# Kernel tuning notes

Measured on AMD Instinct MI355X. Metric: run time of the kernel, lower is better.

Reference implementation:

```python
import jax, jax.numpy as jnp
import numpy as np

NB_CLASSES = 10
EPS = 1e-8  # torch cosine_similarity eps


def gcn_conv(x, W, b, src, dst, n):
    h = x @ W
    deg = jax.ops.segment_sum(jnp.ones_like(src, dtype=h.dtype), dst, num_segments=n) + 1.0
    dinv = deg ** -0.5
    coef = (dinv[src] * dinv[dst])[:, None]
    agg = jax.ops.segment_sum(h[src] * coef, dst, num_segments=n)
    return agg + h * (1.0 / deg)[:, None] + b


def condition_net(e, w_in, b_in, w_hid, b_hid, w_out, b_out):
    # ConditionNet with num_layers=2: input_fc -> elu -> hidden_fc[0] -> elu -> output_fc
    h = jax.nn.elu(e @ w_in + b_in)
    h = jax.nn.elu(h @ w_hid + b_hid)
    return h @ w_out + b_out


def setup_inputs() -> dict:
    key = jax.random.key(0)
    N, E, D, H, T, M = 20000, 320000, 256, 256, 3, 2048
    ks = jax.random.split(key, 24)
    s = 1.0 / np.sqrt(D)
    inp = {
        "x": jax.random.normal(ks[0], (N, D), dtype=jnp.float32),
        "src": jax.random.randint(ks[1], (E,), 0, N, dtype=jnp.int32),
        "dst": jax.random.randint(ks[2], (E,), 0, N, dtype=jnp.int32),
        "idx": jax.random.randint(ks[3], (M,), 0, N, dtype=jnp.int32),
        "labels": jax.random.randint(ks[4], (M,), 0, NB_CLASSES, dtype=jnp.int32),
        "train": 1,
        # 3 GCNConv layers (all D->D, residual structure forces equal widths)
        "gcn_W1": jax.random.normal(ks[5], (D, D), dtype=jnp.float32) * s,
        "gcn_b1": jnp.zeros((D,), dtype=jnp.float32),
        "gcn_W2": jax.random.normal(ks[6], (D, D), dtype=jnp.float32) * s,
        "gcn_b2": jnp.zeros((D,), dtype=jnp.float32),
        "gcn_W3": jax.random.normal(ks[7], (D, D), dtype=jnp.float32) * s,
        "gcn_b3": jnp.zeros((D,), dtype=jnp.float32),
        # T=3 ConditionNets, params stacked on leading axis
        "cn_w_in": jax.random.normal(ks[8], (T, D, H), dtype=jnp.float32) * s,
        "cn_b_in": jnp.zeros((T, H), dtype=jnp.float32),
        "cn_w_hid": jax.random.normal(ks[9], (T, H, H), dtype=jnp.float32) * s,
        "cn_b_hid": jnp.zeros((T, H), dtype=jnp.float32),
        "cn_w_out": jax.random.normal(ks[10], (T, H, D), dtype=jnp.float32) * s,
        "cn_b_out": jnp.zeros((T, D), dtype=jnp.float32),
        # Embed_prompt
        "p_list": jax.random.normal(ks[11], (5, D), dtype=jnp.float32) * s,
        "a_W": jax.random.normal(ks[12], (D, 5), dtype=jnp.float32) * s,
        "a_b": jnp.zeros((5,), dtype=jnp.float32),
        # gcn_weight2 (trainable); weight1 and weight3 are frozen zeros, closed over
        "gcn_weight2": jnp.float32(1.0),
    }
    return inp


def reference(x, src, dst, idx, labels, train,
              gcn_W1, gcn_b1, gcn_W2, gcn_b2, gcn_W3, gcn_b3,
              cn_w_in, cn_b_in, cn_w_hid, cn_b_hid, cn_w_out, cn_b_out,
              p_list, a_W, a_b, gcn_weight2):
    n = x.shape[0]
    origin_x = x
    w1 = jnp.float32(0.0)  # gcn_weight1 (frozen)
    w3 = jnp.float32(0.0)  # gcn_weight3 (frozen)
    T = cn_w_in.shape[0]
    for t in range(T):  # think layers (small static count)
        e1 = gcn_conv(x, gcn_W1, gcn_b1, src, dst, n)
        e2 = gcn_conv(e1, gcn_W2, gcn_b2, src, dst, n) + e1
        e3 = gcn_conv(e2, gcn_W3, gcn_b3, src, dst, n) + e2
        embed = w1 * e1 + gcn_weight2 * e2 + w3 * e3
        prompt = condition_net(embed, cn_w_in[t], cn_b_in[t], cn_w_hid[t], cn_b_hid[t],
                               cn_w_out[t], cn_b_out[t])
        x = prompt * origin_x
    # full gcn(x, edge_index): 3 convs with ELU activation (standard GCN forward)
    h = jax.nn.elu(gcn_conv(x, gcn_W1, gcn_b1, src, dst, n))
    h = jax.nn.elu(gcn_conv(h, gcn_W2, gcn_b2, src, dst, n))
    h = jax.nn.elu(gcn_conv(h, gcn_W3, gcn_b3, src, dst, n))
    # Embed_prompt: attention over 5 learned prompt vectors
    weight = jax.nn.softmax(h @ a_W + a_b, axis=1)  # [N, 5]
    embed = h + weight @ p_list
    rawret = embed[idx]  # [M, D]
    # train==1: class prototypes via scatter-mean over labels
    sums = jax.ops.segment_sum(rawret, labels, num_segments=NB_CLASSES)
    counts = jax.ops.segment_sum(jnp.ones_like(labels, dtype=rawret.dtype), labels,
                                 num_segments=NB_CLASSES)
    ave = sums / jnp.maximum(counts, 1.0)[:, None]  # [C, D]
    # fused cosine similarity: normalize both, one matmul (replaces M*C scalar loop)
    rn = rawret / jnp.maximum(jnp.linalg.norm(rawret, axis=1, keepdims=True), EPS)
    an = ave / jnp.maximum(jnp.linalg.norm(ave, axis=1, keepdims=True), EPS)
    ret = jax.nn.softmax(rn @ an.T, axis=1)  # [M, C]
    return ret
```

## Files before the change

kernel.cpp:

```cpp
#include <hip/hip_runtime.h>
#include <hip/hip_bf16.h>
#include <math.h>

#define NN 20000
#define DD 256
#define EE 320000
#define MM 2048
#define CC 10
#define TT 3

typedef __attribute__((ext_vector_type(8))) short s8v;
typedef __attribute__((ext_vector_type(4))) float f4v;

__device__ unsigned short g_xb[NN * DD];
__device__ unsigned short g_xo[NN * DD];
__device__ unsigned short g_hb[NN * DD];
__device__ unsigned short g_e1b[NN * DD];
__device__ unsigned short g_e2b[NN * DD];
__device__ int   g_cnt[NN];
__device__ int   g_cursor[NN];
__device__ int   g_rowstart[NN + 1];
__device__ float g_dinv[NN];
__device__ float g_invdeg[NN];
__device__ int   g_part[128];
__device__ int2  g_edge[EE];
__device__ float g_sums[CC * DD];
__device__ float g_cntf[CC];
__device__ unsigned short g_wT1[12 * DD * DD];
__device__ unsigned short g_wT2[12 * DD * DD];

__device__ __forceinline__ float wave_sum(float v) {
#pragma unroll
  for (int off = 32; off > 0; off >>= 1) v += __shfl_xor(v, off);
  return v;
}

__device__ __forceinline__ float eluf(float x) {
  return x > 0.f ? x : expm1f(x);
}

__device__ __forceinline__ float bf2f(unsigned short u) {
  union { unsigned int i; float f; } c;
  c.i = (unsigned int)u << 16;
  return c.f;
}

__device__ __forceinline__ float2 bfpair(unsigned int d) {
  union { unsigned int i; float f; } a, b;
  a.i = d << 16;
  b.i = d & 0xffff0000u;
  return make_float2(a.f, b.f);
}

__device__ __forceinline__ unsigned int packbf(float x, float y) {
  union { __hip_bfloat162 v; unsigned int u; } c;
  c.v = __float22bfloat162_rn(make_float2(x, y));
  return c.u;
}

__device__ __forceinline__ void gl_lds16(const unsigned short* g, unsigned short* l) {
  __builtin_amdgcn_global_load_lds(
      (const __attribute__((address_space(1))) unsigned int*)g,
      (__attribute__((address_space(3))) unsigned int*)l, 16, 0, 0);
}

struct WPtrs { const float* p[12]; };

__global__ __launch_bounds__(256) void init_k(const float* __restrict__ x,
                                              unsigned short* __restrict__ xb,
                                              WPtrs wp) {
  __shared__ float t[64][65];
  int b = blockIdx.x;
  int tid = threadIdx.x;
  if (b < 2500) {
    int i = b * 256 + tid;
    const float4* x4 = (const float4*)x;
    float4 a = x4[i * 2], bb = x4[i * 2 + 1];
    uint4 o;
    o.x = packbf(a.x, a.y);
    o.y = packbf(a.z, a.w);
    o.z = packbf(bb.x, bb.y);
    o.w = packbf(bb.z, bb.w);
    ((uint4*)xb)[i] = o;
  } else if (b < 2692) {
    int bb = b - 2500;
    int widx = bb >> 4;
    int rem = bb & 15;
    int kt0 = (rem >> 2) * 64, nt0 = (rem & 3) * 64;
    const float* W = wp.p[widx];
    int ln = tid & 63, lk = tid >> 6;
    for (int kk = lk; kk < 64; kk += 4)
      t[kk][ln] = W[(size_t)(kt0 + kk) * DD + nt0 + ln];
    __syncthreads();
    for (int nn = lk; nn < 64; nn += 4) {
      float v = t[ln][nn];
      __hip_bfloat16 hb = __float2bfloat16(v);
      float hf = __bfloat162float(hb);
      __hip_bfloat16 lb = __float2bfloat16(v - hf);
      union { __hip_bfloat16 b; unsigned short s; } ch, cl;
      ch.b = hb; cl.b = lb;
      size_t o = (size_t)widx * DD * DD + (size_t)(nt0 + nn) * DD + kt0 + ln;
      g_wT1[o] = ch.s;
      g_wT2[o] = cl.s;
    }
  } else {
    int i = (b - 2692) * 256 + tid;
    if (i < NN) { g_cnt[i] = 0; g_cursor[i] = 0; }
    if (i < CC * DD) g_sums[i] = 0.f;
    if (i < CC) g_cntf[i] = 0.f;
  }
}

__global__ void hist_k(const int* __restrict__ dst) {
  int e = blockIdx.x * blockDim.x + threadIdx.x;
  if (e < EE) atomicAdd(&g_cnt[dst[e]], 1);
}

__global__ __launch_bounds__(256) void scanA_k() {
  __shared__ int s[256];
  int t = threadIdx.x;
  int i = blockIdx.x * 256 + t;
  int v = (i < NN) ? g_cnt[i] : 0;
  s[t] = v;
  __syncthreads();
#pragma unroll
  for (int off = 128; off > 0; off >>= 1) {
    if (t < off) s[t] += s[t + off];
    __syncthreads();
  }
  if (t == 0) g_part[blockIdx.x] = s[0];
}

__global__ __launch_bounds__(256) void scanC_k() {
  __shared__ int ps[128];
  __shared__ int s[256];
  int t = threadIdx.x;
  if (t < 128) ps[t] = (t < 79) ? g_part[t] : 0;
  __syncthreads();
#pragma unroll
  for (int off = 1; off < 128; off <<= 1) {
    int v = (t >= off && t < 128) ? ps[t - off] : 0;
    __syncthreads();
    if (t < 128) ps[t] += v;
    __syncthreads();
  }
  int base = (blockIdx.x == 0) ? 0 : ps[blockIdx.x - 1];
  int i = blockIdx.x * 256 + t;
  int v = (i < NN) ? g_cnt[i] : 0;
  s[t] = v;
  __syncthreads();
#pragma unroll
  for (int off = 1; off < 256; off <<= 1) {
    int x2 = (t >= off) ? s[t - off] : 0;
    __syncthreads();
    s[t] += x2;
    __syncthreads();
  }
  if (i < NN) {
    g_rowstart[i] = base + s[t] - v;
    float dg = (float)(v + 1);
    g_invdeg[i] = 1.0f / dg;
    g_dinv[i] = 1.0f / sqrtf(dg);
  }
  if (blockIdx.x == 78 && t == 0) g_rowstart[NN] = EE;
}

__global__ void fill_k(const int* __restrict__ src, const int* __restrict__ dst) {
  int e = blockIdx.x * blockDim.x + threadIdx.x;
  if (e < EE) {
    int d = dst[e];
    int p = atomicAdd(&g_cursor[d], 1);
    int j = g_rowstart[d] + p;
    int si = src[e];
    float coef = g_dinv[si] * g_dinv[d];
    g_edge[j] = make_int2(si * 512, __float_as_int(coef));
  }
}

template <int SPLIT>
union GemmSM {
  unsigned short st[2][(1024 + 512 * SPLIT) * 8];
  float ct[64][68];
};

template <int EPI, int SPLIT>
__global__ __launch_bounds__(256) void gemm_k(const unsigned short* __restrict__ A,
                                              const unsigned short* __restrict__ B1,
                                              const unsigned short* __restrict__ B2,
                                              unsigned short* __restrict__ C,
                                              const float* __restrict__ bias,
                                              const float* __restrict__ alphap,
                                              const unsigned short* __restrict__ mul) {
  __shared__ GemmSM<SPLIT> sm;
  constexpr int CB = 1024 + 512 * SPLIT;
  int b = blockIdx.x;
  int xcd = b & 7, off = b >> 3;
  int logical = (xcd < 4) ? xcd * 157 + off : 628 + (xcd - 4) * 156 + off;
  int mblk = logical >> 2, nblk = logical & 3;
  int row0 = mblk * 64, col0 = nblk * 64;

  int tid = threadIdx.x;
  int wv = tid >> 6, lane = tid & 63;
  int wm = wv >> 1, wn = wv & 1;
  int lr = lane & 15, lk = lane >> 4;

  f4v acc[2][2];
#pragma unroll
  for (int i = 0; i < 2; ++i)
#pragma unroll
    for (int j = 0; j < 2; ++j) acc[i][j] = (f4v){0.f, 0.f, 0.f, 0.f};

  auto stage = [&](int buf, int kt) {
    unsigned short* base = sm.st[buf];
#pragma unroll
    for (int i = 0; i < CB / 256; ++i) {
      int cb = (wv * (CB / 256) + i) * 64;
      int c = cb + lane;
      unsigned short* ldst = base + (size_t)cb * 8;
      if (c < 512) {
        int row = c >> 3, pos = c & 7;
        int kc = pos ^ (row & 7);
        int gr = row0 + row;
        gr = gr < NN ? gr : NN - 1;
        gl_lds16(A + (size_t)gr * DD + kt + kc * 8, ldst);
      } else if (c < 1024) {
        int c2 = c - 512;
        int col = c2 >> 3, pos = c2 & 7;
        int kc = pos ^ (col & 7);
        gl_lds16(B1 + (size_t)(col0 + col) * DD + kt + kc * 8, ldst);
      } else {
        int c2 = c - 1024;
        int col = c2 >> 3, pos = c2 & 7;
        int kc = pos ^ (col & 7);
        gl_lds16(B2 + (size_t)(col0 + col) * DD + kt + kc * 8, ldst);
      }
    }
  };

  stage(0, 0);
  __syncthreads();

  int buf = 0;
#pragma unroll
  for (int t = 0; t < 4; ++t) {
    if (t < 3) stage(buf ^ 1, (t + 1) * 64);
    const unsigned short* base = sm.st[buf];
#pragma unroll
    for (int ksub = 0; ksub < 2; ++ksub) {
      int kc = ksub * 4 + lk;
      s8v a[2], b1v[2], b2v[2];
#pragma unroll
      for (int mi = 0; mi < 2; ++mi) {
        int row = wm * 32 + mi * 16 + lr;
        a[mi] = *(const s8v*)(base + (row * 8 + (kc ^ (row & 7))) * 8);
      }
#pragma unroll
      for (int nj = 0; nj < 2; ++nj) {
        int col = wn * 32 + nj * 16 + lr;
        int ch = col * 8 + (kc ^ (col & 7));
        b1v[nj] = *(const s8v*)(base + (512 + ch) * 8);
        if (SPLIT) b2v[nj] = *(const s8v*)(base + (1024 + ch) * 8);
      }
#pragma unroll
      for (int mi = 0; mi < 2; ++mi)
#pragma unroll
        for (int nj = 0; nj < 2; ++nj) {
          acc[mi][nj] = __builtin_amdgcn_mfma_f32_16x16x32_bf16(a[mi], b1v[nj], acc[mi][nj], 0, 0, 0);
          if (SPLIT)
            acc[mi][nj] = __builtin_amdgcn_mfma_f32_16x16x32_bf16(a[mi], b2v[nj], acc[mi][nj], 0, 0, 0);
        }
    }
    __syncthreads();
    buf ^= 1;
  }

#pragma unroll
  for (int mi = 0; mi < 2; ++mi)
#pragma unroll
    for (int nj = 0; nj < 2; ++nj)
#pragma unroll
      for (int r = 0; r < 4; ++r)
        sm.ct[wm * 32 + mi * 16 + lk * 4 + r][wn * 32 + nj * 16 + lr] = acc[mi][nj][r];
  __syncthreads();

  float alpha = 1.f;
  if (EPI == 1) alpha = alphap ? *alphap : 1.f;
#pragma unroll
  for (int p = 0; p < 2; ++p) {
    int row = p * 32 + (tid >> 3);
    int c0 = (tid & 7) * 8;
    int gr = row0 + row;
    int gc = col0 + c0;
    if (gr < NN) {
      float v[8];
      float4 va = *(float4*)&sm.ct[row][c0];
      float4 vb = *(float4*)&sm.ct[row][c0 + 4];
      v[0] = va.x; v[1] = va.y; v[2] = va.z; v[3] = va.w;
      v[4] = vb.x; v[5] = vb.y; v[6] = vb.z; v[7] = vb.w;
      if (EPI == 1) {
        float4 bv0 = *(const float4*)(bias + gc);
        float4 bv1 = *(const float4*)(bias + gc + 4);
        float bb[8] = {bv0.x, bv0.y, bv0.z, bv0.w, bv1.x, bv1.y, bv1.z, bv1.w};
#pragma unroll
        for (int i = 0; i < 8; ++i) v[i] = eluf(fmaf(alpha, v[i], bb[i]));
      } else if (EPI == 2) {
        float4 bv0 = *(const float4*)(bias + gc);
        float4 bv1 = *(const float4*)(bias + gc + 4);
        float bb[8] = {bv0.x, bv0.y, bv0.z, bv0.w, bv1.x, bv1.y, bv1.z, bv1.w};
        uint4 mu = *(const uint4*)(mul + (size_t)gr * DD + gc);
        float2 m0 = bfpair(mu.x), m1 = bfpair(mu.y), m2 = bfpair(mu.z), m3 = bfpair(mu.w);
        float mm[8] = {m0.x, m0.y, m1.x, m1.y, m2.x, m2.y, m3.x, m3.y};
#pragma unroll
        for (int i = 0; i < 8; ++i) v[i] = (v[i] + bb[i]) * mm[i];
      }
      uint4 o;
      o.x = packbf(v[0], v[1]);
      o.y = packbf(v[2], v[3]);
      o.z = packbf(v[4], v[5]);
      o.w = packbf(v[6], v[7]);
      *(uint4*)(C + (size_t)gr * DD + gc) = o;
    }
  }
}

template <int RES>
__device__ __forceinline__ void agg_row8(int row, int sl, int hf,
                                         const unsigned short* __restrict__ h,
                                         const float* __restrict__ bias,
                                         const unsigned short* __restrict__ res,
                                         float* o) {
  const char* hb = (const char*)h;
  int lo = sl * 16;
  float acc[8];
#pragma unroll
  for (int k = 0; k < 8; ++k) acc[k] = 0.f;
  int s = g_rowstart[row], e = g_rowstart[row + 1];
  int j = s;
  for (; j + 12 <= e; j += 12) {
    int2 E[6];
    uint4 V[6];
#pragma unroll
    for (int u = 0; u < 6; ++u) E[u] = g_edge[j + 2 * u + hf];
#pragma unroll
    for (int u = 0; u < 6; ++u) V[u] = *(const uint4*)(hb + (size_t)E[u].x + lo);
#pragma unroll
    for (int u = 0; u < 6; ++u) {
      float c = __int_as_float(E[u].y);
      float2 p0 = bfpair(V[u].x), p1 = bfpair(V[u].y);
      float2 p2 = bfpair(V[u].z), p3 = bfpair(V[u].w);
      acc[0] = fmaf(c, p0.x, acc[0]); acc[1] = fmaf(c, p0.y, acc[1]);
      acc[2] = fmaf(c, p1.x, acc[2]); acc[3] = fmaf(c, p1.y, acc[3]);
      acc[4] = fmaf(c, p2.x, acc[4]); acc[5] = fmaf(c, p2.y, acc[5]);
      acc[6] = fmaf(c, p3.x, acc[6]); acc[7] = fmaf(c, p3.y, acc[7]);
    }
  }
  for (; j < e; j += 2) {
    int jj = j + hf;
    int jc = jj < e ? jj : e - 1;
    int2 E0 = g_edge[jc];
    uint4 V0 = *(const uint4*)(hb + (size_t)E0.x + lo);
    float c = (jj < e) ? __int_as_float(E0.y) : 0.f;
    float2 p0 = bfpair(V0.x), p1 = bfpair(V0.y);
    float2 p2 = bfpair(V0.z), p3 = bfpair(V0.w);
    acc[0] = fmaf(c, p0.x, acc[0]); acc[1] = fmaf(c, p0.y, acc[1]);
    acc[2] = fmaf(c, p1.x, acc[2]); acc[3] = fmaf(c, p1.y, acc[3]);
    acc[4] = fmaf(c, p2.x, acc[4]); acc[5] = fmaf(c, p2.y, acc[5]);
    acc[6] = fmaf(c, p3.x, acc[6]); acc[7] = fmaf(c, p3.y, acc[7]);
  }
#pragma unroll
  for (int k = 0; k < 8; ++k) acc[k] += __shfl_xor(acc[k], 32);
  float idg = g_invdeg[row];
  uint4 hv = *(const uint4*)(hb + (size_t)row * 512 + lo);
  float2 h0 = bfpair(hv.x), h1 = bfpair(hv.y), h2 = bfpair(hv.z), h3 = bfpair(hv.w);
  float hw[8] = {h0.x, h0.y, h1.x, h1.y, h2.x, h2.y, h3.x, h3.y};
  float4 b0 = *(const float4*)(bias + sl * 8);
  float4 b1 = *(const float4*)(bias + sl * 8 + 4);
  float bb[8] = {b0.x, b0.y, b0.z, b0.w, b1.x, b1.y, b1.z, b1.w};
#pragma unroll
  for (int k = 0; k < 8; ++k) o[k] = acc[k] + hw[k] * idg + bb[k];
  if (RES) {
    uint4 rv = *(const uint4*)((const char*)res + (size_t)row * 512 + lo);
    float2 r0 = bfpair(rv.x), r1 = bfpair(rv.y), r2 = bfpair(rv.z), r3 = bfpair(rv.w);
    float rw[8] = {r0.x, r0.y, r1.x, r1.y, r2.x, r2.y, r3.x, r3.y};
#pragma unroll
    for (int k = 0; k < 8; ++k) o[k] += rw[k];
  }
}

template <int ELU, int RES>
__global__ __launch_bounds__(256) void agg_k(const unsigned short* __restrict__ h,
                                             const float* __restrict__ bias,
                                             const unsigned short* __restrict__ res,
                                             unsigned short* __restrict__ out) {
  int row = (blockIdx.x * 256 + threadIdx.x) >> 6;
  int lane = threadIdx.x & 63;
  int sl = lane & 31, hf = lane >> 5;
  float o[8];
  agg_row8<RES>(row, sl, hf, h, bias, res, o);
  if (ELU) {
#pragma unroll
    for (int k = 0; k < 8; ++k) o[k] = eluf(o[k]);
  }
  if (hf == 0) {
    uint4 pk;
    pk.x = packbf(o[0], o[1]);
    pk.y = packbf(o[2], o[3]);
    pk.z = packbf(o[4], o[5]);
    pk.w = packbf(o[6], o[7]);
    *(uint4*)((char*)out + (size_t)row * 512 + sl * 16) = pk;
  }
}

__global__ __launch_bounds__(256) void aggattn_k(const unsigned short* __restrict__ h,
                                                 const float* __restrict__ bias,
                                                 const float* __restrict__ aW,
                                                 const float* __restrict__ ab,
                                                 const float* __restrict__ plist,
                                                 unsigned short* __restrict__ out) {
  int row = (blockIdx.x * 256 + threadIdx.x) >> 6;
  int lane = threadIdx.x & 63;
  int sl = lane & 31, hf = lane >> 5;
  float o[8];
  agg_row8<0>(row, sl, hf, h, bias, nullptr, o);
#pragma unroll
  for (int k = 0; k < 8; ++k) o[k] = eluf(o[k]);
  int c0 = sl * 8;
  float lg[5];
#pragma unroll
  for (int k = 0; k < 5; ++k) {
    float p = 0.f;
#pragma unroll
    for (int i = 0; i < 8; ++i) p = fmaf(o[i], aW[(c0 + i) * 5 + k], p);
    lg[k] = wave_sum(p) * 0.5f + ab[k];
  }
  float mx = lg[0];
#pragma unroll
  for (int k = 1; k < 5; ++k) mx = fmaxf(mx, lg[k]);
  float w[5], sum = 0.f;
#pragma unroll
  for (int k = 0; k < 5; ++k) { w[k] = expf(lg[k] - mx); sum += w[k]; }
  float inv = 1.f / sum;
#pragma unroll
  for (int k = 0; k < 5; ++k) {
    float wk = w[k] * inv;
    float4 p0 = *(const float4*)(plist + k * DD + c0);
    float4 p1 = *(const float4*)(plist + k * DD + c0 + 4);
    o[0] = fmaf(wk, p0.x, o[0]); o[1] = fmaf(wk, p0.y, o[1]);
    o[2] = fmaf(wk, p0.z, o[2]); o[3] = fmaf(wk, p0.w, o[3]);
    o[4] = fmaf(wk, p1.x, o[4]); o[5] = fmaf(wk, p1.y, o[5]);
    o[6] = fmaf(wk, p1.z, o[6]); o[7] = fmaf(wk, p1.w, o[7]);
  }
  if (hf == 0) {
    uint4 pk;
    pk.x = packbf(o[0], o[1]);
    pk.y = packbf(o[2], o[3]);
    pk.z = packbf(o[4], o[5]);
    pk.w = packbf(o[6], o[7]);
    *(uint4*)((char*)out + (size_t)row * 512 + sl * 16) = pk;
  }
}

__global__ __launch_bounds__(256) void proto_k(const unsigned short* __restrict__ embed,
                                               const int* __restrict__ idxp,
                                               const int* __restrict__ labels) {
  __shared__ float sums[CC][DD];
  __shared__ float cnts[CC];
  int t = threadIdx.x;
#pragma unroll
  for (int c = 0; c < CC; ++c) sums[c][t] = 0.f;
  if (t < CC) cnts[t] = 0.f;
  __syncthreads();
  int m0 = blockIdx.x * 32;
  for (int r0 = 0; r0 < 32; r0 += 4) {
    int i4[4], l4[4];
    float v[4];
#pragma unroll
    for (int u = 0; u < 4; ++u) {
      int m = m0 + r0 + u;
      i4[u] = idxp[m];
      l4[u] = labels[m];
    }
#pragma unroll
    for (int u = 0; u < 4; ++u) v[u] = bf2f(embed[(size_t)i4[u] * DD + t]);
#pragma unroll
    for (int u = 0; u < 4; ++u) sums[l4[u]][t] += v[u];
    if (t == 0) {
#pragma unroll
      for (int u = 0; u < 4; ++u) cnts[l4[u]] += 1.f;
    }
  }
  __syncthreads();
#pragma unroll
  for (int c = 0; c < CC; ++c) atomicAdd(&g_sums[c * DD + t], sums[c][t]);
  if (t < CC) atomicAdd(&g_cntf[t], cnts[t]);
}

__global__ __launch_bounds__(256) void cos_k(const unsigned short* __restrict__ embed,
                                             const int* __restrict__ idxp,
                                             float* __restrict__ out) {
  __shared__ float an[CC][DD];
  __shared__ float red[4];
  int t = threadIdx.x;
  int lane = t & 63, wv = t >> 6;
  for (int c = 0; c < CC; ++c) {
    float v = g_sums[c * DD + t] / fmaxf(g_cntf[c], 1.0f);
    float sq = wave_sum(v * v);
    if (lane == 0) red[wv] = sq;
    __syncthreads();
    float tot = red[0] + red[1] + red[2] + red[3];
    float nrm = fmaxf(sqrtf(tot), 1e-8f);
    an[c][t] = v / nrm;
    __syncthreads();
  }
  int wid = (blockIdx.x * 256 + t) >> 6;
  if (wid >= MM) return;
  int row = idxp[wid];
  uint2 rv = ((const uint2*)embed)[(size_t)row * 64 + lane];
  float2 r0 = bfpair(rv.x), r1 = bfpair(rv.y);
  float4 r = make_float4(r0.x, r0.y, r1.x, r1.y);
  float n = wave_sum(r.x * r.x + r.y * r.y + r.z * r.z + r.w * r.w);
  float rnf = 1.0f / fmaxf(sqrtf(n), 1e-8f);
  float lg[CC];
#pragma unroll
  for (int c = 0; c < CC; ++c) {
    float4 a = ((const float4*)&an[c][0])[lane];
    float p = r.x * a.x + r.y * a.y + r.z * a.z + r.w * a.w;
    lg[c] = wave_sum(p) * rnf;
  }
  float mx = lg[0];
#pragma unroll
  for (int c = 1; c < CC; ++c) mx = fmaxf(mx, lg[c]);
  float s = 0.f, w[CC];
#pragma unroll
  for (int c = 0; c < CC; ++c) { w[c] = expf(lg[c] - mx); s += w[c]; }
  float inv = 1.f / s;
#pragma unroll
  for (int c = 0; c < CC; ++c)
    if (lane == c) out[(size_t)wid * CC + c] = w[c] * inv;
}

extern "C" void kernel_launch(void* const* d_in, const int* in_sizes, int n_in,
                              void* d_out, int out_size, void* d_ws, size_t ws_size,
                              hipStream_t stream) {
  (void)in_sizes; (void)n_in; (void)d_ws; (void)ws_size; (void)out_size;
  const float* x      = (const float*)d_in[0];
  const int*   src    = (const int*)d_in[1];
  const int*   dst    = (const int*)d_in[2];
  const int*   idx    = (const int*)d_in[3];
  const int*   labels = (const int*)d_in[4];
  const float* W1 = (const float*)d_in[6];
  const float* b1 = (const float*)d_in[7];
  const float* W2 = (const float*)d_in[8];
  const float* b2 = (const float*)d_in[9];
  const float* W3 = (const float*)d_in[10];
  const float* b3 = (const float*)d_in[11];
  const float* cw_in  = (const float*)d_in[12];
  const float* cb_in  = (const float*)d_in[13];
  const float* cw_hid = (const float*)d_in[14];
  const float* cb_hid = (const float*)d_in[15];
  const float* cw_out = (const float*)d_in[16];
  const float* cb_out = (const float*)d_in[17];
  const float* plist  = (const float*)d_in[18];
  const float* aW     = (const float*)d_in[19];
  const float* ab     = (const float*)d_in[20];
  const float* w2s    = (const float*)d_in[21];
  float* out = (float*)d_out;

  unsigned short *xb, *xo, *hb, *e1b, *e2b, *wt1, *wt2;
  hipGetSymbolAddress((void**)&xb,  HIP_SYMBOL(g_xb));
  hipGetSymbolAddress((void**)&xo,  HIP_SYMBOL(g_xo));
  hipGetSymbolAddress((void**)&hb,  HIP_SYMBOL(g_hb));
  hipGetSymbolAddress((void**)&e1b, HIP_SYMBOL(g_e1b));
  hipGetSymbolAddress((void**)&e2b, HIP_SYMBOL(g_e2b));
  hipGetSymbolAddress((void**)&wt1, HIP_SYMBOL(g_wT1));
  hipGetSymbolAddress((void**)&wt2, HIP_SYMBOL(g_wT2));

  auto WT1 = [&](int w) { return (const unsigned short*)(wt1 + (size_t)w * DD * DD); };
  auto WT2 = [&](int w) { return (const unsigned short*)(wt2 + (size_t)w * DD * DD); };

  WPtrs wp;
  wp.p[0] = W1; wp.p[1] = W2; wp.p[2] = W3;
  for (int t = 0; t < 3; ++t) {
    wp.p[3 + t] = cw_in  + (size_t)t * DD * DD;
    wp.p[6 + t] = cw_hid + (size_t)t * DD * DD;
    wp.p[9 + t] = cw_out + (size_t)t * DD * DD;
  }
  init_k<<<2771, 256, 0, stream>>>(x, xb, wp);
  hist_k<<<1250, 256, 0, stream>>>(dst);
  scanA_k<<<79, 256, 0, stream>>>();
  scanC_k<<<79, 256, 0, stream>>>();
  fill_k<<<1250, 256, 0, stream>>>(src, dst);

  const int GG = 1252;
  const unsigned short* xin = xb;
  for (int t = 0; t < TT; ++t) {
    gemm_k<0, 1><<<GG, 256, 0, stream>>>(xin, WT1(0), WT2(0), hb, nullptr, nullptr, nullptr);
    agg_k<0, 0><<<5000, 256, 0, stream>>>(hb, b1, nullptr, e1b);
    gemm_k<0, 1><<<GG, 256, 0, stream>>>(e1b, WT1(1), WT2(1), hb, nullptr, nullptr, nullptr);
    agg_k<0, 1><<<5000, 256, 0, stream>>>(hb, b2, e1b, e2b);
    gemm_k<1, 0><<<GG, 256, 0, stream>>>(e2b, WT1(3 + t), WT1(3 + t), e1b,
                                         cb_in + (size_t)t * DD, w2s, nullptr);
    gemm_k<1, 0><<<GG, 256, 0, stream>>>(e1b, WT1(6 + t), WT1(6 + t), hb,
                                         cb_hid + (size_t)t * DD, nullptr, nullptr);
    gemm_k<2, 0><<<GG, 256, 0, stream>>>(hb, WT1(9 + t), WT1(9 + t), xo,
                                         cb_out + (size_t)t * DD, nullptr, xb);
    xin = xo;
  }

  gemm_k<0, 1><<<GG, 256, 0, stream>>>(xin, WT1(0), WT2(0), hb, nullptr, nullptr, nullptr);
  agg_k<1, 0><<<5000, 256, 0, stream>>>(hb, b1, nullptr, e1b);
  gemm_k<0, 1><<<GG, 256, 0, stream>>>(e1b, WT1(1), WT2(1), hb, nullptr, nullptr, nullptr);
  agg_k<1, 0><<<5000, 256, 0, stream>>>(hb, b2, nullptr, e2b);
  gemm_k<0, 1><<<GG, 256, 0, stream>>>(e2b, WT1(2), WT2(2), hb, nullptr, nullptr, nullptr);
  aggattn_k<<<5000, 256, 0, stream>>>(hb, b3, aW, ab, plist, e2b);

  proto_k<<<64, 256, 0, stream>>>(e2b, idx, labels);
  cos_k<<<512, 256, 0, stream>>>(e2b, idx, out);
}
```

Before: 539.3 us.

## Slice GCN aggregation by feature columns and apply prompt attention only to sampled rows

New measurement: 1.017 ms. 1.89x slower.

```diff
diff --git a/kernel.cpp b/kernel.cpp
--- a/kernel.cpp
+++ b/kernel.cpp
@@ -37,12 +37,6 @@
 
 __device__ __forceinline__ float eluf(float x) {
   return x > 0.f ? x : expm1f(x);
-}
-
-__device__ __forceinline__ float bf2f(unsigned short u) {
-  union { unsigned int i; float f; } c;
-  c.i = (unsigned int)u << 16;
-  return c.f;
 }
 
 __device__ __forceinline__ float2 bfpair(unsigned int d) {
@@ -323,115 +317,91 @@
   }
 }
 
-template <int RES>
-__device__ __forceinline__ void agg_row8(int row, int sl, int hf,
-                                         const unsigned short* __restrict__ h,
-                                         const float* __restrict__ bias,
-                                         const unsigned short* __restrict__ res,
-                                         float* o) {
-  const char* hb = (const char*)h;
-  int lo = sl * 16;
-  float acc[8];
-#pragma unroll
-  for (int k = 0; k < 8; ++k) acc[k] = 0.f;
-  int s = g_rowstart[row], e = g_rowstart[row + 1];
-  int j = s;
-  for (; j + 12 <= e; j += 12) {
-    int2 E[6];
-    uint4 V[6];
-#pragma unroll
-    for (int u = 0; u < 6; ++u) E[u] = g_edge[j + 2 * u + hf];
-#pragma unroll
-    for (int u = 0; u < 6; ++u) V[u] = *(const uint4*)(hb + (size_t)E[u].x + lo);
-#pragma unroll
-    for (int u = 0; u < 6; ++u) {
-      float c = __int_as_float(E[u].y);
-      float2 p0 = bfpair(V[u].x), p1 = bfpair(V[u].y);
-      float2 p2 = bfpair(V[u].z), p3 = bfpair(V[u].w);
-      acc[0] = fmaf(c, p0.x, acc[0]); acc[1] = fmaf(c, p0.y, acc[1]);
-      acc[2] = fmaf(c, p1.x, acc[2]); acc[3] = fmaf(c, p1.y, acc[3]);
-      acc[4] = fmaf(c, p2.x, acc[4]); acc[5] = fmaf(c, p2.y, acc[5]);
-      acc[6] = fmaf(c, p3.x, acc[6]); acc[7] = fmaf(c, p3.y, acc[7]);
-    }
-  }
-  for (; j < e; j += 2) {
-    int jj = j + hf;
-    int jc = jj < e ? jj : e - 1;
-    int2 E0 = g_edge[jc];
-    uint4 V0 = *(const uint4*)(hb + (size_t)E0.x + lo);
-    float c = (jj < e) ? __int_as_float(E0.y) : 0.f;
-    float2 p0 = bfpair(V0.x), p1 = bfpair(V0.y);
-    float2 p2 = bfpair(V0.z), p3 = bfpair(V0.w);
-    acc[0] = fmaf(c, p0.x, acc[0]); acc[1] = fmaf(c, p0.y, acc[1]);
-    acc[2] = fmaf(c, p1.x, acc[2]); acc[3] = fmaf(c, p1.y, acc[3]);
-    acc[4] = fmaf(c, p2.x, acc[4]); acc[5] = fmaf(c, p2.y, acc[5]);
-    acc[6] = fmaf(c, p3.x, acc[6]); acc[7] = fmaf(c, p3.y, acc[7]);
-  }
-#pragma unroll
-  for (int k = 0; k < 8; ++k) acc[k] += __shfl_xor(acc[k], 32);
-  float idg = g_invdeg[row];
-  uint4 hv = *(const uint4*)(hb + (size_t)row * 512 + lo);
-  float2 h0 = bfpair(hv.x), h1 = bfpair(hv.y), h2 = bfpair(hv.z), h3 = bfpair(hv.w);
-  float hw[8] = {h0.x, h0.y, h1.x, h1.y, h2.x, h2.y, h3.x, h3.y};
-  float4 b0 = *(const float4*)(bias + sl * 8);
-  float4 b1 = *(const float4*)(bias + sl * 8 + 4);
-  float bb[8] = {b0.x, b0.y, b0.z, b0.w, b1.x, b1.y, b1.z, b1.w};
-#pragma unroll
-  for (int k = 0; k < 8; ++k) o[k] = acc[k] + hw[k] * idg + bb[k];
-  if (RES) {
-    uint4 rv = *(const uint4*)((const char*)res + (size_t)row * 512 + lo);
-    float2 r0 = bfpair(rv.x), r1 = bfpair(rv.y), r2 = bfpair(rv.z), r3 = bfpair(rv.w);
-    float rw[8] = {r0.x, r0.y, r1.x, r1.y, r2.x, r2.y, r3.x, r3.y};
-#pragma unroll
-    for (int k = 0; k < 8; ++k) o[k] += rw[k];
-  }
-}
-
 template <int ELU, int RES>
 __global__ __launch_bounds__(256) void agg_k(const unsigned short* __restrict__ h,
                                              const float* __restrict__ bias,
                                              const unsigned short* __restrict__ res,
                                              unsigned short* __restrict__ out) {
-  int row = (blockIdx.x * 256 + threadIdx.x) >> 6;
-  int lane = threadIdx.x & 63;
-  int sl = lane & 31, hf = lane >> 5;
-  float o[8];
-  agg_row8<RES>(row, sl, hf, h, bias, res, o);
-  if (ELU) {
-#pragma unroll
-    for (int k = 0; k < 8; ++k) o[k] = eluf(o[k]);
-  }
-  if (hf == 0) {
-    uint4 pk;
-    pk.x = packbf(o[0], o[1]);
-    pk.y = packbf(o[2], o[3]);
-    pk.z = packbf(o[4], o[5]);
-    pk.w = packbf(o[6], o[7]);
-    *(uint4*)((char*)out + (size_t)row * 512 + sl * 16) = pk;
-  }
-}
-
-__global__ __launch_bounds__(256) void aggattn_k(const unsigned short* __restrict__ h,
-                                                 const float* __restrict__ bias,
-                                                 const float* __restrict__ aW,
-                                                 const float* __restrict__ ab,
-                                                 const float* __restrict__ plist,
-                                                 unsigned short* __restrict__ out) {
-  int row = (blockIdx.x * 256 + threadIdx.x) >> 6;
-  int lane = threadIdx.x & 63;
-  int sl = lane & 31, hf = lane >> 5;
-  float o[8];
-  agg_row8<0>(row, sl, hf, h, bias, nullptr, o);
-#pragma unroll
-  for (int k = 0; k < 8; ++k) o[k] = eluf(o[k]);
-  int c0 = sl * 8;
+  int b = blockIdx.x;
+  int slice = b & 7, chunk = b >> 3;
+  int t = threadIdx.x;
+  int wv = t >> 6, lane = t & 63;
+  int g = lane >> 4, sl = lane & 15;
+  int lo = slice * 64 + sl * 4;
+  const char* hb8 = (const char*)h;
+  float2 bv = *(const float2*)(bias + slice * 32 + sl * 2);
+  int rbase = chunk * 64 + wv * 16;
+#pragma unroll 1
+  for (int rr = 0; rr < 16; ++rr) {
+    int row = rbase + rr;
+    if (row >= NN) break;
+    int s = g_rowstart[row], e = g_rowstart[row + 1];
+    float ax = 0.f, ay = 0.f;
+    int j = s;
+    for (; j + 16 <= e; j += 16) {
+      int2 E[4];
+      unsigned int V[4];
+#pragma unroll
+      for (int u = 0; u < 4; ++u) E[u] = g_edge[j + u * 4 + g];
+#pragma unroll
+      for (int u = 0; u < 4; ++u) V[u] = *(const unsigned int*)(hb8 + (size_t)E[u].x + lo);
+#pragma unroll
+      for (int u = 0; u < 4; ++u) {
+        float c = __int_as_float(E[u].y);
+        float2 p = bfpair(V[u]);
+        ax = fmaf(c, p.x, ax);
+        ay = fmaf(c, p.y, ay);
+      }
+    }
+    for (; j + 4 <= e; j += 4) {
+      int2 E0 = g_edge[j + g];
+      unsigned int V0 = *(const unsigned int*)(hb8 + (size_t)E0.x + lo);
+      float c = __int_as_float(E0.y);
+      float2 p = bfpair(V0);
+      ax = fmaf(c, p.x, ax);
+      ay = fmaf(c, p.y, ay);
+    }
+    if (j < e) {
+      int jj = j + g;
+      if (jj < e) {
+        int2 E0 = g_edge[jj];
+        unsigned int V0 = *(const unsigned int*)(hb8 + (size_t)E0.x + lo);
+        float c = __int_as_float(E0.y);
+        float2 p = bfpair(V0);
+        ax = fmaf(c, p.x, ax);
+        ay = fmaf(c, p.y, ay);
+      }
+    }
+    ax += __shfl_xor(ax, 16); ax += __shfl_xor(ax, 32);
+    ay += __shfl_xor(ay, 16); ay += __shfl_xor(ay, 32);
+    float idg = g_invdeg[row];
+    unsigned int hv = *(const unsigned int*)(hb8 + (size_t)row * 512 + lo);
+    float2 hp = bfpair(hv);
+    float ox = ax + hp.x * idg + bv.x;
+    float oy = ay + hp.y * idg + bv.y;
+    if (RES) {
+      unsigned int rv = *(const unsigned int*)((const char*)res + (size_t)row * 512 + lo);
+      float2 rp = bfpair(rv);
+      ox += rp.x;
+      oy += rp.y;
+    }
+    if (ELU) { ox = eluf(ox); oy = eluf(oy); }
+    if (g == 0)
+      *(unsigned int*)((char*)out + (size_t)row * 512 + lo) = packbf(ox, oy);
+  }
+}
+
+__device__ __forceinline__ float4 attn_apply(float4 r, int lane,
+                                             const float* __restrict__ aW,
+                                             const float* __restrict__ ab,
+                                             const float* __restrict__ plist) {
+  int d = lane * 4;
   float lg[5];
 #pragma unroll
   for (int k = 0; k < 5; ++k) {
-    float p = 0.f;
-#pragma unroll
-    for (int i = 0; i < 8; ++i) p = fmaf(o[i], aW[(c0 + i) * 5 + k], p);
-    lg[k] = wave_sum(p) * 0.5f + ab[k];
+    float p = r.x * aW[(d + 0) * 5 + k] + r.y * aW[(d + 1) * 5 + k] +
+              r.z * aW[(d + 2) * 5 + k] + r.w * aW[(d + 3) * 5 + k];
+    lg[k] = wave_sum(p) + ab[k];
   }
   float mx = lg[0];
 #pragma unroll
@@ -443,26 +413,21 @@
 #pragma unroll
   for (int k = 0; k < 5; ++k) {
     float wk = w[k] * inv;
-    float4 p0 = *(const float4*)(plist + k * DD + c0);
-    float4 p1 = *(const float4*)(plist + k * DD + c0 + 4);
-    o[0] = fmaf(wk, p0.x, o[0]); o[1] = fmaf(wk, p0.y, o[1]);
-    o[2] = fmaf(wk, p0.z, o[2]); o[3] = fmaf(wk, p0.w, o[3]);
-    o[4] = fmaf(wk, p1.x, o[4]); o[5] = fmaf(wk, p1.y, o[5]);
-    o[6] = fmaf(wk, p1.z, o[6]); o[7] = fmaf(wk, p1.w, o[7]);
-  }
-  if (hf == 0) {
-    uint4 pk;
-    pk.x = packbf(o[0], o[1]);
-    pk.y = packbf(o[2], o[3]);
-    pk.z = packbf(o[4], o[5]);
-    pk.w = packbf(o[6], o[7]);
-    *(uint4*)((char*)out + (size_t)row * 512 + sl * 16) = pk;
-  }
-}
-
-__global__ __launch_bounds__(256) void proto_k(const unsigned short* __restrict__ embed,
+    float4 pv = *(const float4*)(plist + k * DD + d);
+    r.x = fmaf(wk, pv.x, r.x);
+    r.y = fmaf(wk, pv.y, r.y);
+    r.z = fmaf(wk, pv.z, r.z);
+    r.w = fmaf(wk, pv.w, r.w);
+  }
+  return r;
+}
+
+__global__ __launch_bounds__(256) void proto_k(const unsigned short* __restrict__ h,
                                                const int* __restrict__ idxp,
-                                               const int* __restrict__ labels) {
+                                               const int* __restrict__ labels,
+                                               const float* __restrict__ aW,
+                                               const float* __restrict__ ab,
+                                               const float* __restrict__ plist) {
   __shared__ float sums[CC][DD];
   __shared__ float cnts[CC];
   int t = threadIdx.x;
@@ -470,24 +435,21 @@
   for (int c = 0; c < CC; ++c) sums[c][t] = 0.f;
   if (t < CC) cnts[t] = 0.f;
   __syncthreads();
-  int m0 = blockIdx.x * 32;
-  for (int r0 = 0; r0 < 32; r0 += 4) {
-    int i4[4], l4[4];
-    float v[4];
-#pragma unroll
-    for (int u = 0; u < 4; ++u) {
-      int m = m0 + r0 + u;
-      i4[u] = idxp[m];
-      l4[u] = labels[m];
-    }
-#pragma unroll
-    for (int u = 0; u < 4; ++u) v[u] = bf2f(embed[(size_t)i4[u] * DD + t]);
-#pragma unroll
-    for (int u = 0; u < 4; ++u) sums[l4[u]][t] += v[u];
-    if (t == 0) {
-#pragma unroll
-      for (int u = 0; u < 4; ++u) cnts[l4[u]] += 1.f;
-    }
+  int wv = t >> 6, lane = t & 63;
+  int m0 = blockIdx.x * 64 + wv * 16;
+  int d = lane * 4;
+  for (int rr = 0; rr < 16; ++rr) {
+    int m = m0 + rr;
+    int row = idxp[m];
+    int lab = labels[m];
+    uint2 rv = *(const uint2*)((const char*)h + (size_t)row * 512 + lane * 8);
+    float2 a0 = bfpair(rv.x), a1 = bfpair(rv.y);
+    float4 r = attn_apply(make_float4(a0.x, a0.y, a1.x, a1.y), lane, aW, ab, plist);
+    atomicAdd(&sums[lab][d + 0], r.x);
+    atomicAdd(&sums[lab][d + 1], r.y);
+    atomicAdd(&sums[lab][d + 2], r.z);
+    atomicAdd(&sums[lab][d + 3], r.w);
+    if (lane == 0) atomicAdd(&cnts[lab], 1.f);
   }
   __syncthreads();
 #pragma unroll
@@ -495,8 +457,11 @@
   if (t < CC) atomicAdd(&g_cntf[t], cnts[t]);
 }
 
-__global__ __launch_bounds__(256) void cos_k(const unsigned short* __restrict__ embed,
+__global__ __launch_bounds__(256) void cos_k(const unsigned short* __restrict__ h,
                                              const int* __restrict__ idxp,
+                                             const float* __restrict__ aW,
+                                             const float* __restrict__ ab,
+                                             const float* __restrict__ plist,
                                              float* __restrict__ out) {
   __shared__ float an[CC][DD];
   __shared__ float red[4];
@@ -515,9 +480,9 @@
   int wid = (blockIdx.x * 256 + t) >> 6;
   if (wid >= MM) return;
   int row = idxp[wid];
-  uint2 rv = ((const uint2*)embed)[(size_t)row * 64 + lane];
+  uint2 rv = *(const uint2*)((const char*)h + (size_t)row * 512 + lane * 8);
   float2 r0 = bfpair(rv.x), r1 = bfpair(rv.y);
-  float4 r = make_float4(r0.x, r0.y, r1.x, r1.y);
+  float4 r = attn_apply(make_float4(r0.x, r0.y, r1.x, r1.y), lane, aW, ab, plist);
   float n = wave_sum(r.x * r.x + r.y * r.y + r.z * r.z + r.w * r.w);
   float rnf = 1.0f / fmaxf(sqrtf(n), 1e-8f);
   float lg[CC];
@@ -592,12 +557,13 @@
   fill_k<<<1250, 256, 0, stream>>>(src, dst);
 
   const int GG = 1252;
+  const int GA = 2504;
   const unsigned short* xin = xb;
   for (int t = 0; t < TT; ++t) {
     gemm_k<0, 1><<<GG, 256, 0, stream>>>(xin, WT1(0), WT2(0), hb, nullptr, nullptr, nullptr);
-    agg_k<0, 0><<<5000, 256, 0, stream>>>(hb, b1, nullptr, e1b);
+    agg_k<0, 0><<<GA, 256, 0, stream>>>(hb, b1, nullptr, e1b);
     gemm_k<0, 1><<<GG, 256, 0, stream>>>(e1b, WT1(1), WT2(1), hb, nullptr, nullptr, nullptr);
-    agg_k<0, 1><<<5000, 256, 0, stream>>>(hb, b2, e1b, e2b);
+    agg_k<0, 1><<<GA, 256, 0, stream>>>(hb, b2, e1b, e2b);
     gemm_k<1, 0><<<GG, 256, 0, stream>>>(e2b, WT1(3 + t), WT1(3 + t), e1b,
                                          cb_in + (size_t)t * DD, w2s, nullptr);
     gemm_k<1, 0><<<GG, 256, 0, stream>>>(e1b, WT1(6 + t), WT1(6 + t), hb,
@@ -608,12 +574,12 @@
   }
 
   gemm_k<0, 1><<<GG, 256, 0, stream>>>(xin, WT1(0), WT2(0), hb, nullptr, nullptr, nullptr);
-  agg_k<1, 0><<<5000, 256, 0, stream>>>(hb, b1, nullptr, e1b);
+  agg_k<1, 0><<<GA, 256, 0, stream>>>(hb, b1, nullptr, e1b);
   gemm_k<0, 1><<<GG, 256, 0, stream>>>(e1b, WT1(1), WT2(1), hb, nullptr, nullptr, nullptr);
-  agg_k<1, 0><<<5000, 256, 0, stream>>>(hb, b2, nullptr, e2b);
+  agg_k<1, 0><<<GA, 256, 0, stream>>>(hb, b2, nullptr, e2b);
   gemm_k<0, 1><<<GG, 256, 0, stream>>>(e2b, WT1(2), WT2(2), hb, nullptr, nullptr, nullptr);
-  aggattn_k<<<5000, 256, 0, stream>>>(hb, b3, aW, ab, plist, e2b);
-
-  proto_k<<<64, 256, 0, stream>>>(e2b, idx, labels);
-  cos_k<<<512, 256, 0, stream>>>(e2b, idx, out);
-}
+  agg_k<1, 0><<<GA, 256, 0, stream>>>(hb, b3, nullptr, e1b);
+
+  proto_k<<<32, 256, 0, stream>>>(e1b, idx, labels, aW, ab, plist);
+  cos_k<<<512, 256, 0, stream>>>(e1b, idx, aW, ab, plist, out);
+}
```

## Compute prompt attention only for the sampled rows inside proto and cos kernels

Applied to the files above, without the earlier changes.

Result: slower. 556.8 us (+3.3%).

```diff
diff --git a/kernel.cpp b/kernel.cpp
--- a/kernel.cpp
+++ b/kernel.cpp
@@ -37,12 +37,6 @@
 
 __device__ __forceinline__ float eluf(float x) {
   return x > 0.f ? x : expm1f(x);
-}
-
-__device__ __forceinline__ float bf2f(unsigned short u) {
-  union { unsigned int i; float f; } c;
-  c.i = (unsigned int)u << 16;
-  return c.f;
 }
 
 __device__ __forceinline__ float2 bfpair(unsigned int d) {
@@ -411,27 +405,17 @@
   }
 }
 
-__global__ __launch_bounds__(256) void aggattn_k(const unsigned short* __restrict__ h,
-                                                 const float* __restrict__ bias,
-                                                 const float* __restrict__ aW,
-                                                 const float* __restrict__ ab,
-                                                 const float* __restrict__ plist,
-                                                 unsigned short* __restrict__ out) {
-  int row = (blockIdx.x * 256 + threadIdx.x) >> 6;
-  int lane = threadIdx.x & 63;
-  int sl = lane & 31, hf = lane >> 5;
-  float o[8];
-  agg_row8<0>(row, sl, hf, h, bias, nullptr, o);
-#pragma unroll
-  for (int k = 0; k < 8; ++k) o[k] = eluf(o[k]);
-  int c0 = sl * 8;
+__device__ __forceinline__ float4 attn_apply(float4 r, int lane,
+                                             const float* __restrict__ aW,
+                                             const float* __restrict__ ab,
+                                             const float* __restrict__ plist) {
+  int d = lane * 4;
   float lg[5];
 #pragma unroll
   for (int k = 0; k < 5; ++k) {
-    float p = 0.f;
-#pragma unroll
-    for (int i = 0; i < 8; ++i) p = fmaf(o[i], aW[(c0 + i) * 5 + k], p);
-    lg[k] = wave_sum(p) * 0.5f + ab[k];
+    float p = r.x * aW[(d + 0) * 5 + k] + r.y * aW[(d + 1) * 5 + k] +
+              r.z * aW[(d + 2) * 5 + k] + r.w * aW[(d + 3) * 5 + k];
+    lg[k] = wave_sum(p) + ab[k];
   }
   float mx = lg[0];
 #pragma unroll
@@ -443,26 +427,21 @@
 #pragma unroll
   for (int k = 0; k < 5; ++k) {
     float wk = w[k] * inv;
-    float4 p0 = *(const float4*)(plist + k * DD + c0);
-    float4 p1 = *(const float4*)(plist + k * DD + c0 + 4);
-    o[0] = fmaf(wk, p0.x, o[0]); o[1] = fmaf(wk, p0.y, o[1]);
-    o[2] = fmaf(wk, p0.z, o[2]); o[3] = fmaf(wk, p0.w, o[3]);
-    o[4] = fmaf(wk, p1.x, o[4]); o[5] = fmaf(wk, p1.y, o[5]);
-    o[6] = fmaf(wk, p1.z, o[6]); o[7] = fmaf(wk, p1.w, o[7]);
-  }
-  if (hf == 0) {
-    uint4 pk;
-    pk.x = packbf(o[0], o[1]);
-    pk.y = packbf(o[2], o[3]);
-    pk.z = packbf(o[4], o[5]);
-    pk.w = packbf(o[6], o[7]);
-    *(uint4*)((char*)out + (size_t)row * 512 + sl * 16) = pk;
-  }
-}
-
-__global__ __launch_bounds__(256) void proto_k(const unsigned short* __restrict__ embed,
+    float4 pv = *(const float4*)(plist + k * DD + d);
+    r.x = fmaf(wk, pv.x, r.x);
+    r.y = fmaf(wk, pv.y, r.y);
+    r.z = fmaf(wk, pv.z, r.z);
+    r.w = fmaf(wk, pv.w, r.w);
+  }
+  return r;
+}
+
+__global__ __launch_bounds__(256) void proto_k(const unsigned short* __restrict__ h,
                                                const int* __restrict__ idxp,
-                                               const int* __restrict__ labels) {
+                                               const int* __restrict__ labels,
+                                               const float* __restrict__ aW,
+                                               const float* __restrict__ ab,
+                                               const float* __restrict__ plist) {
   __shared__ float sums[CC][DD];
   __shared__ float cnts[CC];
   int t = threadIdx.x;
@@ -470,24 +449,21 @@
   for (int c = 0; c < CC; ++c) sums[c][t] = 0.f;
   if (t < CC) cnts[t] = 0.f;
   __syncthreads();
-  int m0 = blockIdx.x * 32;
-  for (int r0 = 0; r0 < 32; r0 += 4) {
-    int i4[4], l4[4];
-    float v[4];
-#pragma unroll
-    for (int u = 0; u < 4; ++u) {
-      int m = m0 + r0 + u;
-      i4[u] = idxp[m];
-      l4[u] = labels[m];
-    }
-#pragma unroll
-    for (int u = 0; u < 4; ++u) v[u] = bf2f(embed[(size_t)i4[u] * DD + t]);
-#pragma unroll
-    for (int u = 0; u < 4; ++u) sums[l4[u]][t] += v[u];
-    if (t == 0) {
-#pragma unroll
-      for (int u = 0; u < 4; ++u) cnts[l4[u]] += 1.f;
-    }
+  int wv = t >> 6, lane = t & 63;
+  int m0 = blockIdx.x * 64 + wv * 16;
+  int d = lane * 4;
+  for (int rr = 0; rr < 16; ++rr) {
+    int m = m0 + rr;
+    int row = idxp[m];
+    int lab = labels[m];
+    uint2 rv = *(const uint2*)((const char*)h + (size_t)row * 512 + lane * 8);
+    float2 a0 = bfpair(rv.x), a1 = bfpair(rv.y);
+    float4 r = attn_apply(make_float4(a0.x, a0.y, a1.x, a1.y), lane, aW, ab, plist);
+    atomicAdd(&sums[lab][d + 0], r.x);
+    atomicAdd(&sums[lab][d + 1], r.y);
+    atomicAdd(&sums[lab][d + 2], r.z);
+    atomicAdd(&sums[lab][d + 3], r.w);
+    if (lane == 0) atomicAdd(&cnts[lab], 1.f);
   }
   __syncthreads();
 #pragma unroll
@@ -495,8 +471,11 @@
   if (t < CC) atomicAdd(&g_cntf[t], cnts[t]);
 }
 
-__global__ __launch_bounds__(256) void cos_k(const unsigned short* __restrict__ embed,
+__global__ __launch_bounds__(256) void cos_k(const unsigned short* __restrict__ h,
                                              const int* __restrict__ idxp,
+                                             const float* __restrict__ aW,
+                                             const float* __restrict__ ab,
+                                             const float* __restrict__ plist,
                                              float* __restrict__ out) {
   __shared__ float an[CC][DD];
   __shared__ float red[4];
@@ -515,9 +494,9 @@
   int wid = (blockIdx.x * 256 + t) >> 6;
   if (wid >= MM) return;
   int row = idxp[wid];
-  uint2 rv = ((const uint2*)embed)[(size_t)row * 64 + lane];
+  uint2 rv = *(const uint2*)((const char*)h + (size_t)row * 512 + lane * 8);
   float2 r0 = bfpair(rv.x), r1 = bfpair(rv.y);
-  float4 r = make_float4(r0.x, r0.y, r1.x, r1.y);
+  float4 r = attn_apply(make_float4(r0.x, r0.y, r1.x, r1.y), lane, aW, ab, plist);
   float n = wave_sum(r.x * r.x + r.y * r.y + r.z * r.z + r.w * r.w);
   float rnf = 1.0f / fmaxf(sqrtf(n), 1e-8f);
   float lg[CC];
@@ -612,8 +591,8 @@
   gemm_k<0, 1><<<GG, 256, 0, stream>>>(e1b, WT1(1), WT2(1), hb, nullptr, nullptr, nullptr);
   agg_k<1, 0><<<5000, 256, 0, stream>>>(hb, b2, nullptr, e2b);
   gemm_k<0, 1><<<GG, 256, 0, stream>>>(e2b, WT1(2), WT2(2), hb, nullptr, nullptr, nullptr);
-  aggattn_k<<<5000, 256, 0, stream>>>(hb, b3, aW, ab, plist, e2b);
-
-  proto_k<<<64, 256, 0, stream>>>(e2b, idx, labels);
-  cos_k<<<512, 256, 0, stream>>>(e2b, idx, out);
-}
+  agg_k<1, 0><<<5000, 256, 0, stream>>>(hb, b3, nullptr, e1b);
+
+  proto_k<<<32, 256, 0, stream>>>(e1b, idx, labels, aW, ab, plist);
+  cos_k<<<512, 256, 0, stream>>>(e1b, idx, aW, ab, plist, out);
+}
```
